# Kernel optimization log

Hardware: AMD Instinct MI355X
Metric: run time of the kernel (lower is better)

## Reference

```python
import jax, jax.numpy as jnp
import numpy as np

B, C, N, K = 2, 64, 20000, 16
COUT = 64


def setup_inputs() -> dict:
    key = jax.random.key(0)
    k1, k2, k3, k4, k5 = jax.random.split(key, 5)
    x = jax.random.normal(k1, (B, C, N, 1), dtype=jnp.float32)
    edge_index = jax.random.randint(k2, (2, B, N, K), 0, N)
    pos = jax.random.normal(k3, (B, 3, N, 1), dtype=jnp.float32)
    # BasicConv([2C, COUT]) -> 1x1 Conv2d weight [COUT, 2C] (+bias), then ReLU
    W = jax.random.normal(k4, (COUT, 2 * C), dtype=jnp.float32) * (1.0 / np.sqrt(2 * C))
    b = jax.random.normal(k5, (COUT,), dtype=jnp.float32) * 0.01
    return {"x": x, "edge_index": edge_index, "pos": pos, "W": W, "b": b}


def _gather(t, idx):
    # t: [B, C, N, 1], idx: [B, N, K] -> [B, C, N, K]
    t3 = t[..., 0]  # [B, C, N]
    return jax.vmap(lambda tb, ib: tb[:, ib])(t3, idx)


def reference(x, edge_index, pos, W, b):
    x_i = _gather(x, edge_index[1])           # [B, C, N, K] center
    x_j = _gather(x, edge_index[0])           # [B, C, N, K] neighbor
    feat = jnp.concatenate([x_i, x_j - x_i], axis=1)  # [B, 2C, N, K]
    # 1x1 conv + bias + ReLU
    out = jnp.einsum('oc,bcnk->bonk', W, feat) + b[None, :, None, None]
    out = jax.nn.relu(out)
    # distance-based suppression
    pos_i = _gather(pos, edge_index[1])       # [B, 3, N, K]
    pos_j = _gather(pos, edge_index[0])
    dis = jnp.sqrt(jnp.sum(jnp.square(pos_j - pos_i), axis=1))  # [B, N, K]
    suppression = 2.0 * jax.nn.sigmoid(-dis)[:, None, :, :]     # [B, 1, N, K]
    out = out * suppression
    max_value = jnp.max(out, axis=-1, keepdims=True)             # [B, COUT, N, 1]
    return max_value
```

## Files before the change

### kernel.cpp

```cpp
#include <hip/hip_runtime.h>
#include <math.h>

#define B_    2
#define C_    64
#define N_    20000
#define K_    16
#define COUT_ 64
#define TNC   64
#define NBC   ((N_ + TNC - 1) / TNC)
#define TN    16
#define NB    (N_ / TN)

typedef unsigned int   u32;
typedef unsigned short u16;
typedef __attribute__((ext_vector_type(8))) short bf16x8;
typedef __attribute__((ext_vector_type(4))) float f32x4;

static __device__ __forceinline__ u16 f2bf(float f) {
    union { float f; u32 u; } v; v.f = f;
    u32 r = (v.u + 0x7FFFu + ((v.u >> 16) & 1u)) >> 16;
    return (u16)r;
}
static __device__ __forceinline__ float uasf(u32 u) {
    union { u32 u; float f; } v; v.u = u; return v.f;
}
static __device__ __forceinline__ bf16x8 asbf(uint4 v) {
    union { uint4 u; bf16x8 b; } c; c.u = v; return c.b;
}

__global__ __launch_bounds__(256)
void precast(const float* __restrict__ x, const float* __restrict__ W,
             u16* __restrict__ xb, u16* __restrict__ wfrag) {
    const int bi = blockIdx.x;
    const int t  = threadIdx.x;

    if (bi == B_ * NBC) {
        const int l  = t & 63;
        const int ot = t >> 6;
        const int o  = ot * 16 + (l & 15);
        const int cb = (l >> 4) << 3;
        #pragma unroll
        for (int h = 0; h < 2; ++h) {
            u32 p1[4], p2[4];
            #pragma unroll
            for (int jj = 0; jj < 4; ++jj) {
                int c0 = h * 32 + cb + 2 * jj, c1 = c0 + 1;
                float w1a = W[o * 128 + c0],      w1b = W[o * 128 + c1];
                float w2a = W[o * 128 + 64 + c0], w2b = W[o * 128 + 64 + c1];
                p1[jj] = (u32)f2bf(w1a - w2a) | ((u32)f2bf(w1b - w2b) << 16);
                p2[jj] = (u32)f2bf(w2a)       | ((u32)f2bf(w2b)       << 16);
            }
            *(uint4*)&wfrag[(size_t)((ot * 4 + h)     * 64 + l) * 8] =
                make_uint4(p1[0], p1[1], p1[2], p1[3]);
            *(uint4*)&wfrag[(size_t)((ot * 4 + 2 + h) * 64 + l) * 8] =
                make_uint4(p2[0], p2[1], p2[2], p2[3]);
        }
        return;
    }

    __shared__ float tile[64][68];
    const int b  = bi / NBC;
    const int n0 = (bi % NBC) * TNC;
    const float* xbase = x + (size_t)b * C_ * N_;
    #pragma unroll
    for (int r = 0; r < 4; ++r) {
        int flat = r * 256 + t;
        int c = flat >> 4, ng = (flat & 15) * 4;
        int n = n0 + ng;
        float4 v;
        if (n + 3 < N_) {
            v = *(const float4*)&xbase[c * N_ + n];
        } else {
            v.x = (n     < N_) ? xbase[c * N_ + n    ] : 0.0f;
            v.y = (n + 1 < N_) ? xbase[c * N_ + n + 1] : 0.0f;
            v.z = (n + 2 < N_) ? xbase[c * N_ + n + 2] : 0.0f;
            v.w = (n + 3 < N_) ? xbase[c * N_ + n + 3] : 0.0f;
        }
        *(float4*)&tile[c][ng] = v;
    }
    __syncthreads();

    const int n = t >> 2, q = t & 3;
    if (n0 + n < N_) {
        u32 p[8];
        #pragma unroll
        for (int jj = 0; jj < 8; ++jj) {
            float v0 = tile[q * 16 + 2 * jj][n];
            float v1 = tile[q * 16 + 2 * jj + 1][n];
            p[jj] = (u32)f2bf(v0) | ((u32)f2bf(v1) << 16);
        }
        u16* dst = xb + ((size_t)(b * N_ + n0 + n)) * 64 + q * 16;
        *(uint4*)dst       = make_uint4(p[0], p[1], p[2], p[3]);
        *(uint4*)(dst + 8) = make_uint4(p[4], p[5], p[6], p[7]);
    }
}

__global__ __launch_bounds__(256)
void fused(const int* __restrict__ ei, const float* __restrict__ pos,
           const u16* __restrict__ xb, const u16* __restrict__ wfrag,
           const float* __restrict__ bias, float* __restrict__ out) {
    __shared__ uint2 esl[256];
    __shared__ float otile[16][66];

    const int bi   = blockIdx.x;
    const int b    = bi / NB;
    const int n0   = (bi % NB) * TN;
    const int t    = threadIdx.x;
    const int lane = t & 63;
    const int w    = t >> 6;
    const int g    = lane >> 4;
    const int col  = lane & 15;

    {
        const int idx = n0 * K_ + t;
        int i0 = ei[(size_t)b * N_ * K_ + idx];
        int i1 = ei[((size_t)B_ + b) * N_ * K_ + idx];
        const float* pb = pos + (size_t)b * 3 * N_;
        float dx = pb[i0]          - pb[i1];
        float dy = pb[N_ + i0]     - pb[N_ + i1];
        float dz = pb[2 * N_ + i0] - pb[2 * N_ + i1];
        float dis = sqrtf(dx * dx + dy * dy + dz * dz);
        float s = 2.0f / (1.0f + __expf(dis));
        esl[t] = make_uint2((u32)i0 | ((u32)i1 << 16), __float_as_uint(s));
    }

    bf16x8 wf[16];
    #pragma unroll
    for (int f = 0; f < 16; ++f)
        wf[f] = *(const bf16x8*)&wfrag[(size_t)(f * 64 + lane) * 8];
    const float bo0 = bias[col], bo1 = bias[16 + col],
                bo2 = bias[32 + col], bo3 = bias[48 + col];
    __syncthreads();

    const uint4* xrow = (const uint4*)(xb + (size_t)b * N_ * 64);

    #pragma unroll
    for (int it = 0; it < 4; ++it) {
        const int nt = it * 4 + w;
        uint2 ee = esl[nt * 16 + col];
        int   i0 = (int)(ee.x & 0xFFFFu);
        int   i1 = (int)(ee.x >> 16);
        const uint4* ri = xrow + ((size_t)i1 << 3);
        const uint4* rj = xrow + ((size_t)i0 << 3);
        bf16x8 xi_lo = asbf(ri[g]);
        bf16x8 xi_hi = asbf(ri[4 + g]);
        bf16x8 xj_lo = asbf(rj[g]);
        bf16x8 xj_hi = asbf(rj[4 + g]);

        f32x4 ac0 = {0,0,0,0}, ac1 = ac0, ac2 = ac0, ac3 = ac0;
        ac0 = __builtin_amdgcn_mfma_f32_16x16x32_bf16(xi_lo, wf[0],  ac0, 0,0,0);
        ac0 = __builtin_amdgcn_mfma_f32_16x16x32_bf16(xi_hi, wf[1],  ac0, 0,0,0);
        ac0 = __builtin_amdgcn_mfma_f32_16x16x32_bf16(xj_lo, wf[2],  ac0, 0,0,0);
        ac0 = __builtin_amdgcn_mfma_f32_16x16x32_bf16(xj_hi, wf[3],  ac0, 0,0,0);
        ac1 = __builtin_amdgcn_mfma_f32_16x16x32_bf16(xi_lo, wf[4],  ac1, 0,0,0);
        ac1 = __builtin_amdgcn_mfma_f32_16x16x32_bf16(xi_hi, wf[5],  ac1, 0,0,0);
        ac1 = __builtin_amdgcn_mfma_f32_16x16x32_bf16(xj_lo, wf[6],  ac1, 0,0,0);
        ac1 = __builtin_amdgcn_mfma_f32_16x16x32_bf16(xj_hi, wf[7],  ac1, 0,0,0);
        ac2 = __builtin_amdgcn_mfma_f32_16x16x32_bf16(xi_lo, wf[8],  ac2, 0,0,0);
        ac2 = __builtin_amdgcn_mfma_f32_16x16x32_bf16(xi_hi, wf[9],  ac2, 0,0,0);
        ac2 = __builtin_amdgcn_mfma_f32_16x16x32_bf16(xj_lo, wf[10], ac2, 0,0,0);
        ac2 = __builtin_amdgcn_mfma_f32_16x16x32_bf16(xj_hi, wf[11], ac2, 0,0,0);
        ac3 = __builtin_amdgcn_mfma_f32_16x16x32_bf16(xi_lo, wf[12], ac3, 0,0,0);
        ac3 = __builtin_amdgcn_mfma_f32_16x16x32_bf16(xi_hi, wf[13], ac3, 0,0,0);
        ac3 = __builtin_amdgcn_mfma_f32_16x16x32_bf16(xj_lo, wf[14], ac3, 0,0,0);
        ac3 = __builtin_amdgcn_mfma_f32_16x16x32_bf16(xj_hi, wf[15], ac3, 0,0,0);

        float m0 = 0.f, m1 = 0.f, m2 = 0.f, m3 = 0.f;
#define EPI(REG) { \
        float sv = uasf(esl[nt * 16 + g * 4 + REG].y); \
        m0 = fmaxf(m0, fmaxf(ac0[REG] + bo0, 0.f) * sv); \
        m1 = fmaxf(m1, fmaxf(ac1[REG] + bo1, 0.f) * sv); \
        m2 = fmaxf(m2, fmaxf(ac2[REG] + bo2, 0.f) * sv); \
        m3 = fmaxf(m3, fmaxf(ac3[REG] + bo3, 0.f) * sv); }
        EPI(0) EPI(1) EPI(2) EPI(3)
#undef EPI
        m0 = fmaxf(m0, __shfl_xor(m0, 16)); m0 = fmaxf(m0, __shfl_xor(m0, 32));
        m1 = fmaxf(m1, __shfl_xor(m1, 16)); m1 = fmaxf(m1, __shfl_xor(m1, 32));
        m2 = fmaxf(m2, __shfl_xor(m2, 16)); m2 = fmaxf(m2, __shfl_xor(m2, 32));
        m3 = fmaxf(m3, __shfl_xor(m3, 16)); m3 = fmaxf(m3, __shfl_xor(m3, 32));
        if (lane < 16) {
            otile[nt][col]      = m0;
            otile[nt][16 + col] = m1;
            otile[nt][32 + col] = m2;
            otile[nt][48 + col] = m3;
        }
    }
    __syncthreads();

    #pragma unroll
    for (int r = 0; r < 4; ++r) {
        int flat = r * 256 + t;
        int o = flat >> 4, n2 = flat & 15;
        __builtin_nontemporal_store(otile[n2][o],
            &out[((size_t)b * COUT_ + o) * N_ + n0 + n2]);
    }
}

extern "C" void kernel_launch(void* const* d_in, const int* in_sizes, int n_in,
                              void* d_out, int out_size, void* d_ws, size_t ws_size,
                              hipStream_t stream) {
    const float* x    = (const float*)d_in[0];
    const int*   ei   = (const int*)  d_in[1];
    const float* pos  = (const float*)d_in[2];
    const float* W    = (const float*)d_in[3];
    const float* bias = (const float*)d_in[4];
    float*       out  = (float*)d_out;

    u16* xb    = (u16*)d_ws;
    u16* wfrag = xb + (size_t)B_ * N_ * 64;

    hipLaunchKernelGGL(precast, dim3(B_ * NBC + 1), dim3(256), 0, stream,
                       x, W, xb, wfrag);
    hipLaunchKernelGGL(fused, dim3(B_ * NB), dim3(256), 0, stream,
                       ei, pos, xb, wfrag, bias, out);
}
```

Before: 110.7 us.

## Move edge index decode and distance suppression into prep kernel

The per-edge work (reading both edge index arrays, gathering positions, computing distance and sigmoid suppression) moves out of the fused kernel into the prep kernel. Prep now runs a fixed grid of 1024 blocks, and each block also handles a slice of edges. The packed index and suppression records go to a workspace buffer, which the fused kernel then reads with one 64-bit load per thread. This takes the dependent pos gathers off the MFMA kernel's critical path, at the cost of an extra 640 KB intermediate write and read.

New measurement: 118.1 us. +6.7%, slower.

```diff
diff --git a/kernel.cpp b/kernel.cpp
--- a/kernel.cpp
+++ b/kernel.cpp
@@ -10,9 +10,12 @@
 #define NBC   ((N_ + TNC - 1) / TNC)
 #define TN    16
 #define NB    (N_ / TN)
+#define NEDGE (B_ * N_ * K_)
+#define PREPB 1024
 
 typedef unsigned int   u32;
 typedef unsigned short u16;
+typedef unsigned long long u64;
 typedef __attribute__((ext_vector_type(8))) short bf16x8;
 typedef __attribute__((ext_vector_type(4))) float f32x4;
 
@@ -29,12 +32,34 @@
 }
 
 __global__ __launch_bounds__(256)
-void precast(const float* __restrict__ x, const float* __restrict__ W,
-             u16* __restrict__ xb, u16* __restrict__ wfrag) {
-    const int bi = blockIdx.x;
-    const int t  = threadIdx.x;
-
-    if (bi == B_ * NBC) {
+void prep(const float* __restrict__ x, const float* __restrict__ W,
+          const int* __restrict__ ei, const float* __restrict__ pos,
+          u16* __restrict__ xb, u16* __restrict__ wfrag,
+          u64* __restrict__ ebuf) {
+    const int bid = blockIdx.x;
+    const int t   = threadIdx.x;
+
+    {
+        const int base = bid * (NEDGE / PREPB);
+        #pragma unroll
+        for (int k = t; k < NEDGE / PREPB; k += 256) {
+            const int g = base + k;
+            const int b = g / (N_ * K_);
+            int i0 = __builtin_nontemporal_load(&ei[g]);
+            int i1 = __builtin_nontemporal_load(&ei[NEDGE + g]);
+            const float* pb = pos + (size_t)b * 3 * N_;
+            float dx = pb[i0]          - pb[i1];
+            float dy = pb[N_ + i0]     - pb[N_ + i1];
+            float dz = pb[2 * N_ + i0] - pb[2 * N_ + i1];
+            float dis = sqrtf(dx * dx + dy * dy + dz * dz);
+            float s = 2.0f / (1.0f + __expf(dis));
+            u64 rec = (u64)((u32)i0 | ((u32)i1 << 16)) |
+                      ((u64)__float_as_uint(s) << 32);
+            __builtin_nontemporal_store(rec, &ebuf[g]);
+        }
+    }
+
+    if (bid == B_ * NBC) {
         const int l  = t & 63;
         const int ot = t >> 6;
         const int o  = ot * 16 + (l & 15);
@@ -57,10 +82,11 @@
         }
         return;
     }
+    if (bid > B_ * NBC) return;
 
     __shared__ float tile[64][68];
-    const int b  = bi / NBC;
-    const int n0 = (bi % NBC) * TNC;
+    const int b  = bid / NBC;
+    const int n0 = (bid % NBC) * TNC;
     const float* xbase = x + (size_t)b * C_ * N_;
     #pragma unroll
     for (int r = 0; r < 4; ++r) {
@@ -96,9 +122,9 @@
 }
 
 __global__ __launch_bounds__(256)
-void fused(const int* __restrict__ ei, const float* __restrict__ pos,
-           const u16* __restrict__ xb, const u16* __restrict__ wfrag,
-           const float* __restrict__ bias, float* __restrict__ out) {
+void fused2(const u64* __restrict__ ebuf,
+            const u16* __restrict__ xb, const u16* __restrict__ wfrag,
+            const float* __restrict__ bias, float* __restrict__ out) {
     __shared__ uint2 esl[256];
     __shared__ float otile[16][66];
 
@@ -112,16 +138,9 @@
     const int col  = lane & 15;
 
     {
-        const int idx = n0 * K_ + t;
-        int i0 = ei[(size_t)b * N_ * K_ + idx];
-        int i1 = ei[((size_t)B_ + b) * N_ * K_ + idx];
-        const float* pb = pos + (size_t)b * 3 * N_;
-        float dx = pb[i0]          - pb[i1];
-        float dy = pb[N_ + i0]     - pb[N_ + i1];
-        float dz = pb[2 * N_ + i0] - pb[2 * N_ + i1];
-        float dis = sqrtf(dx * dx + dy * dy + dz * dz);
-        float s = 2.0f / (1.0f + __expf(dis));
-        esl[t] = make_uint2((u32)i0 | ((u32)i1 << 16), __float_as_uint(s));
+        u64 rec = __builtin_nontemporal_load(&ebuf[(size_t)b * N_ * K_ +
+                                                   n0 * K_ + t]);
+        esl[t] = make_uint2((u32)rec, (u32)(rec >> 32));
     }
 
     bf16x8 wf[16];
@@ -208,9 +227,10 @@
 
     u16* xb    = (u16*)d_ws;
     u16* wfrag = xb + (size_t)B_ * N_ * 64;
-
-    hipLaunchKernelGGL(precast, dim3(B_ * NBC + 1), dim3(256), 0, stream,
-                       x, W, xb, wfrag);
-    hipLaunchKernelGGL(fused, dim3(B_ * NB), dim3(256), 0, stream,
-                       ei, pos, xb, wfrag, bias, out);
-}
+    u64* ebuf  = (u64*)(wfrag + 64 * 64 * 2);
+
+    hipLaunchKernelGGL(prep, dim3(PREPB), dim3(256), 0, stream,
+                       x, W, ei, pos, xb, wfrag, ebuf);
+    hipLaunchKernelGGL(fused2, dim3(B_ * NB), dim3(256), 0, stream,
+                       ebuf, xb, wfrag, bias, out);
+}
```

## Stage weight fragments in LDS and issue all neighbor gathers upfront

Applied to the files above, without the earlier changes.

Weight fragments are copied into shared memory once per block and read from LDS for each MFMA, replacing the 16 per-lane register-held fragments. All 16 gather loads for the four node tiles are hoisted ahead of any compute, so more memory requests are in flight at once. Launch bounds now request 3 blocks per CU to limit register use. In exchange there are extra LDS reads per MFMA, a 16KB shared allocation per block that may limit occupancy, and higher register pressure from the hoisted loads.

New measurement: 108.1 us. 1.02x faster.

```diff
diff --git a/kernel.cpp b/kernel.cpp
--- a/kernel.cpp
+++ b/kernel.cpp
@@ -95,11 +95,12 @@
     }
 }
 
-__global__ __launch_bounds__(256)
+__global__ __launch_bounds__(256, 3)
 void fused(const int* __restrict__ ei, const float* __restrict__ pos,
            const u16* __restrict__ xb, const u16* __restrict__ wfrag,
            const float* __restrict__ bias, float* __restrict__ out) {
     __shared__ uint2 esl[256];
+    __shared__ u16   wlds[16 * 64 * 8];
     __shared__ float otile[16][66];
 
     const int bi   = blockIdx.x;
@@ -122,69 +123,83 @@
         float dis = sqrtf(dx * dx + dy * dy + dz * dz);
         float s = 2.0f / (1.0f + __expf(dis));
         esl[t] = make_uint2((u32)i0 | ((u32)i1 << 16), __float_as_uint(s));
-    }
-
-    bf16x8 wf[16];
-    #pragma unroll
-    for (int f = 0; f < 16; ++f)
-        wf[f] = *(const bf16x8*)&wfrag[(size_t)(f * 64 + lane) * 8];
+        #pragma unroll
+        for (int r = 0; r < 4; ++r) {
+            int e = r * 256 + t;
+            ((uint4*)wlds)[e] = ((const uint4*)wfrag)[e];
+        }
+    }
     const float bo0 = bias[col], bo1 = bias[16 + col],
                 bo2 = bias[32 + col], bo3 = bias[48 + col];
     __syncthreads();
 
     const uint4* xrow = (const uint4*)(xb + (size_t)b * N_ * 64);
 
-    #pragma unroll
-    for (int it = 0; it < 4; ++it) {
-        const int nt = it * 4 + w;
-        uint2 ee = esl[nt * 16 + col];
-        int   i0 = (int)(ee.x & 0xFFFFu);
-        int   i1 = (int)(ee.x >> 16);
-        const uint4* ri = xrow + ((size_t)i1 << 3);
-        const uint4* rj = xrow + ((size_t)i0 << 3);
-        bf16x8 xi_lo = asbf(ri[g]);
-        bf16x8 xi_hi = asbf(ri[4 + g]);
-        bf16x8 xj_lo = asbf(rj[g]);
-        bf16x8 xj_hi = asbf(rj[4 + g]);
-
-        f32x4 ac0 = {0,0,0,0}, ac1 = ac0, ac2 = ac0, ac3 = ac0;
-        ac0 = __builtin_amdgcn_mfma_f32_16x16x32_bf16(xi_lo, wf[0],  ac0, 0,0,0);
-        ac0 = __builtin_amdgcn_mfma_f32_16x16x32_bf16(xi_hi, wf[1],  ac0, 0,0,0);
-        ac0 = __builtin_amdgcn_mfma_f32_16x16x32_bf16(xj_lo, wf[2],  ac0, 0,0,0);
-        ac0 = __builtin_amdgcn_mfma_f32_16x16x32_bf16(xj_hi, wf[3],  ac0, 0,0,0);
-        ac1 = __builtin_amdgcn_mfma_f32_16x16x32_bf16(xi_lo, wf[4],  ac1, 0,0,0);
-        ac1 = __builtin_amdgcn_mfma_f32_16x16x32_bf16(xi_hi, wf[5],  ac1, 0,0,0);
-        ac1 = __builtin_amdgcn_mfma_f32_16x16x32_bf16(xj_lo, wf[6],  ac1, 0,0,0);
-        ac1 = __builtin_amdgcn_mfma_f32_16x16x32_bf16(xj_hi, wf[7],  ac1, 0,0,0);
-        ac2 = __builtin_amdgcn_mfma_f32_16x16x32_bf16(xi_lo, wf[8],  ac2, 0,0,0);
-        ac2 = __builtin_amdgcn_mfma_f32_16x16x32_bf16(xi_hi, wf[9],  ac2, 0,0,0);
-        ac2 = __builtin_amdgcn_mfma_f32_16x16x32_bf16(xj_lo, wf[10], ac2, 0,0,0);
-        ac2 = __builtin_amdgcn_mfma_f32_16x16x32_bf16(xj_hi, wf[11], ac2, 0,0,0);
-        ac3 = __builtin_amdgcn_mfma_f32_16x16x32_bf16(xi_lo, wf[12], ac3, 0,0,0);
-        ac3 = __builtin_amdgcn_mfma_f32_16x16x32_bf16(xi_hi, wf[13], ac3, 0,0,0);
-        ac3 = __builtin_amdgcn_mfma_f32_16x16x32_bf16(xj_lo, wf[14], ac3, 0,0,0);
-        ac3 = __builtin_amdgcn_mfma_f32_16x16x32_bf16(xj_hi, wf[15], ac3, 0,0,0);
-
-        float m0 = 0.f, m1 = 0.f, m2 = 0.f, m3 = 0.f;
-#define EPI(REG) { \
-        float sv = uasf(esl[nt * 16 + g * 4 + REG].y); \
-        m0 = fmaxf(m0, fmaxf(ac0[REG] + bo0, 0.f) * sv); \
-        m1 = fmaxf(m1, fmaxf(ac1[REG] + bo1, 0.f) * sv); \
-        m2 = fmaxf(m2, fmaxf(ac2[REG] + bo2, 0.f) * sv); \
-        m3 = fmaxf(m3, fmaxf(ac3[REG] + bo3, 0.f) * sv); }
-        EPI(0) EPI(1) EPI(2) EPI(3)
-#undef EPI
-        m0 = fmaxf(m0, __shfl_xor(m0, 16)); m0 = fmaxf(m0, __shfl_xor(m0, 32));
-        m1 = fmaxf(m1, __shfl_xor(m1, 16)); m1 = fmaxf(m1, __shfl_xor(m1, 32));
-        m2 = fmaxf(m2, __shfl_xor(m2, 16)); m2 = fmaxf(m2, __shfl_xor(m2, 32));
-        m3 = fmaxf(m3, __shfl_xor(m3, 16)); m3 = fmaxf(m3, __shfl_xor(m3, 32));
-        if (lane < 16) {
-            otile[nt][col]      = m0;
-            otile[nt][16 + col] = m1;
-            otile[nt][32 + col] = m2;
-            otile[nt][48 + col] = m3;
-        }
-    }
+    uint2 eA = esl[(w)      * 16 + col];
+    uint2 eB = esl[(4 + w)  * 16 + col];
+    uint2 eC = esl[(8 + w)  * 16 + col];
+    uint2 eD = esl[(12 + w) * 16 + col];
+    const uint4* riA = xrow + ((size_t)(eA.x >> 16) << 3);
+    const uint4* rjA = xrow + ((size_t)(eA.x & 0xFFFFu) << 3);
+    const uint4* riB = xrow + ((size_t)(eB.x >> 16) << 3);
+    const uint4* rjB = xrow + ((size_t)(eB.x & 0xFFFFu) << 3);
+    const uint4* riC = xrow + ((size_t)(eC.x >> 16) << 3);
+    const uint4* rjC = xrow + ((size_t)(eC.x & 0xFFFFu) << 3);
+    const uint4* riD = xrow + ((size_t)(eD.x >> 16) << 3);
+    const uint4* rjD = xrow + ((size_t)(eD.x & 0xFFFFu) << 3);
+
+    uint4 A0 = riA[g], A1 = riA[4 + g], A2 = rjA[g], A3 = rjA[4 + g];
+    uint4 B0 = riB[g], B1 = riB[4 + g], B2 = rjB[g], B3 = rjB[4 + g];
+    uint4 C0 = riC[g], C1 = riC[4 + g], C2 = rjC[g], C3 = rjC[4 + g];
+    uint4 D0 = riD[g], D1 = riD[4 + g], D2 = rjD[g], D3 = rjD[4 + g];
+
+#define WF(F) (*(const bf16x8*)&wlds[(size_t)((F) * 64 + lane) * 8])
+
+#define NODE(NT, L0, L1, L2, L3) { \
+    f32x4 ac0 = {0,0,0,0}, ac1 = ac0, ac2 = ac0, ac3 = ac0; \
+    bf16x8 f0 = asbf(L0), f1 = asbf(L1), f2 = asbf(L2), f3 = asbf(L3); \
+    ac0 = __builtin_amdgcn_mfma_f32_16x16x32_bf16(f0, WF(0),  ac0, 0,0,0); \
+    ac0 = __builtin_amdgcn_mfma_f32_16x16x32_bf16(f1, WF(1),  ac0, 0,0,0); \
+    ac0 = __builtin_amdgcn_mfma_f32_16x16x32_bf16(f2, WF(2),  ac0, 0,0,0); \
+    ac0 = __builtin_amdgcn_mfma_f32_16x16x32_bf16(f3, WF(3),  ac0, 0,0,0); \
+    ac1 = __builtin_amdgcn_mfma_f32_16x16x32_bf16(f0, WF(4),  ac1, 0,0,0); \
+    ac1 = __builtin_amdgcn_mfma_f32_16x16x32_bf16(f1, WF(5),  ac1, 0,0,0); \
+    ac1 = __builtin_amdgcn_mfma_f32_16x16x32_bf16(f2, WF(6),  ac1, 0,0,0); \
+    ac1 = __builtin_amdgcn_mfma_f32_16x16x32_bf16(f3, WF(7),  ac1, 0,0,0); \
+    ac2 = __builtin_amdgcn_mfma_f32_16x16x32_bf16(f0, WF(8),  ac2, 0,0,0); \
+    ac2 = __builtin_amdgcn_mfma_f32_16x16x32_bf16(f1, WF(9),  ac2, 0,0,0); \
+    ac2 = __builtin_amdgcn_mfma_f32_16x16x32_bf16(f2, WF(10), ac2, 0,0,0); \
+    ac2 = __builtin_amdgcn_mfma_f32_16x16x32_bf16(f3, WF(11), ac2, 0,0,0); \
+    ac3 = __builtin_amdgcn_mfma_f32_16x16x32_bf16(f0, WF(12), ac3, 0,0,0); \
+    ac3 = __builtin_amdgcn_mfma_f32_16x16x32_bf16(f1, WF(13), ac3, 0,0,0); \
+    ac3 = __builtin_amdgcn_mfma_f32_16x16x32_bf16(f2, WF(14), ac3, 0,0,0); \
+    ac3 = __builtin_amdgcn_mfma_f32_16x16x32_bf16(f3, WF(15), ac3, 0,0,0); \
+    float m0 = 0.f, m1 = 0.f, m2 = 0.f, m3 = 0.f; \
+    _Pragma("unroll") \
+    for (int r4 = 0; r4 < 4; ++r4) { \
+        float sv = uasf(esl[(NT) * 16 + g * 4 + r4].y); \
+        m0 = fmaxf(m0, fmaxf(ac0[r4] + bo0, 0.f) * sv); \
+        m1 = fmaxf(m1, fmaxf(ac1[r4] + bo1, 0.f) * sv); \
+        m2 = fmaxf(m2, fmaxf(ac2[r4] + bo2, 0.f) * sv); \
+        m3 = fmaxf(m3, fmaxf(ac3[r4] + bo3, 0.f) * sv); \
+    } \
+    m0 = fmaxf(m0, __shfl_xor(m0, 16)); m0 = fmaxf(m0, __shfl_xor(m0, 32)); \
+    m1 = fmaxf(m1, __shfl_xor(m1, 16)); m1 = fmaxf(m1, __shfl_xor(m1, 32)); \
+    m2 = fmaxf(m2, __shfl_xor(m2, 16)); m2 = fmaxf(m2, __shfl_xor(m2, 32)); \
+    m3 = fmaxf(m3, __shfl_xor(m3, 16)); m3 = fmaxf(m3, __shfl_xor(m3, 32)); \
+    if (lane < 16) { \
+        otile[NT][col]      = m0; \
+        otile[NT][16 + col] = m1; \
+        otile[NT][32 + col] = m2; \
+        otile[NT][48 + col] = m3; \
+    } }
+
+    NODE(w,      A0, A1, A2, A3)
+    NODE(4 + w,  B0, B1, B2, B3)
+    NODE(8 + w,  C0, C1, C2, C3)
+    NODE(12 + w, D0, D1, D2, D3)
+#undef NODE
+#undef WF
     __syncthreads();
 
     #pragma unroll
```

## Double-buffer gathered features into LDS via async global_load_lds

Applied to the files above, without the earlier changes.

Replaces direct register gathers of neighbor/center feature rows with asynchronous global-to-LDS loads, double-buffered per wave so the next tile's gather overlaps the current tile's MFMAs. Weight fragments and bias are staged in shared memory instead of held in 16 VGPR vectors, reducing register pressure. This adds roughly 40KB of LDS per block, which may reduce occupancy, and relies on hand-placed vmcnt waits for correctness.

Result: slower. 114.9 us (+3.8%).

```diff
diff --git a/kernel.cpp b/kernel.cpp
--- a/kernel.cpp
+++ b/kernel.cpp
@@ -16,6 +16,10 @@
 typedef __attribute__((ext_vector_type(8))) short bf16x8;
 typedef __attribute__((ext_vector_type(4))) float f32x4;
 
+typedef const __attribute__((address_space(1))) void* gas1_t;
+typedef __attribute__((address_space(3)))       void* las3_t;
+#define GL2LDS(g, l) __builtin_amdgcn_global_load_lds((gas1_t)(g), (las3_t)(l), 16, 0, 0)
+
 static __device__ __forceinline__ u16 f2bf(float f) {
     union { float f; u32 u; } v; v.f = f;
     u32 r = (v.u + 0x7FFFu + ((v.u >> 16) & 1u)) >> 16;
@@ -23,9 +27,6 @@
 }
 static __device__ __forceinline__ float uasf(u32 u) {
     union { u32 u; float f; } v; v.u = u; return v.f;
-}
-static __device__ __forceinline__ bf16x8 asbf(uint4 v) {
-    union { uint4 u; bf16x8 b; } c; c.u = v; return c.b;
 }
 
 __global__ __launch_bounds__(256)
@@ -99,7 +100,10 @@
 void fused(const int* __restrict__ ei, const float* __restrict__ pos,
            const u16* __restrict__ xb, const u16* __restrict__ wfrag,
            const float* __restrict__ bias, float* __restrict__ out) {
+    __shared__ u16   feat[4][2][4][512];
+    __shared__ u16   wlds[16 * 64 * 8];
     __shared__ uint2 esl[256];
+    __shared__ float bsl[64];
     __shared__ float otile[16][66];
 
     const int bi   = blockIdx.x;
@@ -122,58 +126,74 @@
         float dis = sqrtf(dx * dx + dy * dy + dz * dz);
         float s = 2.0f / (1.0f + __expf(dis));
         esl[t] = make_uint2((u32)i0 | ((u32)i1 << 16), __float_as_uint(s));
-    }
-
-    bf16x8 wf[16];
-    #pragma unroll
-    for (int f = 0; f < 16; ++f)
-        wf[f] = *(const bf16x8*)&wfrag[(size_t)(f * 64 + lane) * 8];
-    const float bo0 = bias[col], bo1 = bias[16 + col],
-                bo2 = bias[32 + col], bo3 = bias[48 + col];
+        #pragma unroll
+        for (int r = 0; r < 4; ++r) {
+            int e = r * 256 + t;
+            ((uint4*)wlds)[e] = ((const uint4*)wfrag)[e];
+        }
+        if (t < 64) bsl[t] = bias[t];
+    }
     __syncthreads();
 
-    const uint4* xrow = (const uint4*)(xb + (size_t)b * N_ * 64);
-
+    const u16* xbase = xb + (size_t)b * N_ * 64;
+
+    auto issue = [&](int nt, int bf) {
+        uint2 ee = esl[nt * 16 + col];
+        const u16* ri = xbase + ((size_t)(ee.x >> 16) << 6) + g * 8;
+        const u16* rj = xbase + ((size_t)(ee.x & 0xFFFFu) << 6) + g * 8;
+        GL2LDS(ri,      &feat[w][bf][0][0]);
+        GL2LDS(ri + 32, &feat[w][bf][1][0]);
+        GL2LDS(rj,      &feat[w][bf][2][0]);
+        GL2LDS(rj + 32, &feat[w][bf][3][0]);
+    };
+
+#define WF(F) (*(const bf16x8*)&wlds[(size_t)((F) * 64 + lane) * 8])
+
+    const float bo0 = bsl[col], bo1 = bsl[16 + col],
+                bo2 = bsl[32 + col], bo3 = bsl[48 + col];
+
+    issue(w, 0);
     #pragma unroll
     for (int it = 0; it < 4; ++it) {
         const int nt = it * 4 + w;
-        uint2 ee = esl[nt * 16 + col];
-        int   i0 = (int)(ee.x & 0xFFFFu);
-        int   i1 = (int)(ee.x >> 16);
-        const uint4* ri = xrow + ((size_t)i1 << 3);
-        const uint4* rj = xrow + ((size_t)i0 << 3);
-        bf16x8 xi_lo = asbf(ri[g]);
-        bf16x8 xi_hi = asbf(ri[4 + g]);
-        bf16x8 xj_lo = asbf(rj[g]);
-        bf16x8 xj_hi = asbf(rj[4 + g]);
+        const int bf = it & 1;
+        if (it < 3) issue((it + 1) * 4 + w, bf ^ 1);
+        if (it < 3) { asm volatile("s_waitcnt vmcnt(4)" ::: "memory"); }
+        else        { asm volatile("s_waitcnt vmcnt(0)" ::: "memory"); }
+        __builtin_amdgcn_sched_barrier(0);
+
+        bf16x8 f0 = *(const bf16x8*)&feat[w][bf][0][lane * 8];
+        bf16x8 f1 = *(const bf16x8*)&feat[w][bf][1][lane * 8];
+        bf16x8 f2 = *(const bf16x8*)&feat[w][bf][2][lane * 8];
+        bf16x8 f3 = *(const bf16x8*)&feat[w][bf][3][lane * 8];
 
         f32x4 ac0 = {0,0,0,0}, ac1 = ac0, ac2 = ac0, ac3 = ac0;
-        ac0 = __builtin_amdgcn_mfma_f32_16x16x32_bf16(xi_lo, wf[0],  ac0, 0,0,0);
-        ac0 = __builtin_amdgcn_mfma_f32_16x16x32_bf16(xi_hi, wf[1],  ac0, 0,0,0);
-        ac0 = __builtin_amdgcn_mfma_f32_16x16x32_bf16(xj_lo, wf[2],  ac0, 0,0,0);
-        ac0 = __builtin_amdgcn_mfma_f32_16x16x32_bf16(xj_hi, wf[3],  ac0, 0,0,0);
-        ac1 = __builtin_amdgcn_mfma_f32_16x16x32_bf16(xi_lo, wf[4],  ac1, 0,0,0);
-        ac1 = __builtin_amdgcn_mfma_f32_16x16x32_bf16(xi_hi, wf[5],  ac1, 0,0,0);
-        ac1 = __builtin_amdgcn_mfma_f32_16x16x32_bf16(xj_lo, wf[6],  ac1, 0,0,0);
-        ac1 = __builtin_amdgcn_mfma_f32_16x16x32_bf16(xj_hi, wf[7],  ac1, 0,0,0);
-        ac2 = __builtin_amdgcn_mfma_f32_16x16x32_bf16(xi_lo, wf[8],  ac2, 0,0,0);
-        ac2 = __builtin_amdgcn_mfma_f32_16x16x32_bf16(xi_hi, wf[9],  ac2, 0,0,0);
-        ac2 = __builtin_amdgcn_mfma_f32_16x16x32_bf16(xj_lo, wf[10], ac2, 0,0,0);
-        ac2 = __builtin_amdgcn_mfma_f32_16x16x32_bf16(xj_hi, wf[11], ac2, 0,0,0);
-        ac3 = __builtin_amdgcn_mfma_f32_16x16x32_bf16(xi_lo, wf[12], ac3, 0,0,0);
-        ac3 = __builtin_amdgcn_mfma_f32_16x16x32_bf16(xi_hi, wf[13], ac3, 0,0,0);
-        ac3 = __builtin_amdgcn_mfma_f32_16x16x32_bf16(xj_lo, wf[14], ac3, 0,0,0);
-        ac3 = __builtin_amdgcn_mfma_f32_16x16x32_bf16(xj_hi, wf[15], ac3, 0,0,0);
+        ac0 = __builtin_amdgcn_mfma_f32_16x16x32_bf16(f0, WF(0),  ac0, 0,0,0);
+        ac0 = __builtin_amdgcn_mfma_f32_16x16x32_bf16(f1, WF(1),  ac0, 0,0,0);
+        ac0 = __builtin_amdgcn_mfma_f32_16x16x32_bf16(f2, WF(2),  ac0, 0,0,0);
+        ac0 = __builtin_amdgcn_mfma_f32_16x16x32_bf16(f3, WF(3),  ac0, 0,0,0);
+        ac1 = __builtin_amdgcn_mfma_f32_16x16x32_bf16(f0, WF(4),  ac1, 0,0,0);
+        ac1 = __builtin_amdgcn_mfma_f32_16x16x32_bf16(f1, WF(5),  ac1, 0,0,0);
+        ac1 = __builtin_amdgcn_mfma_f32_16x16x32_bf16(f2, WF(6),  ac1, 0,0,0);
+        ac1 = __builtin_amdgcn_mfma_f32_16x16x32_bf16(f3, WF(7),  ac1, 0,0,0);
+        ac2 = __builtin_amdgcn_mfma_f32_16x16x32_bf16(f0, WF(8),  ac2, 0,0,0);
+        ac2 = __builtin_amdgcn_mfma_f32_16x16x32_bf16(f1, WF(9),  ac2, 0,0,0);
+        ac2 = __builtin_amdgcn_mfma_f32_16x16x32_bf16(f2, WF(10), ac2, 0,0,0);
+        ac2 = __builtin_amdgcn_mfma_f32_16x16x32_bf16(f3, WF(11), ac2, 0,0,0);
+        ac3 = __builtin_amdgcn_mfma_f32_16x16x32_bf16(f0, WF(12), ac3, 0,0,0);
+        ac3 = __builtin_amdgcn_mfma_f32_16x16x32_bf16(f1, WF(13), ac3, 0,0,0);
+        ac3 = __builtin_amdgcn_mfma_f32_16x16x32_bf16(f2, WF(14), ac3, 0,0,0);
+        ac3 = __builtin_amdgcn_mfma_f32_16x16x32_bf16(f3, WF(15), ac3, 0,0,0);
 
         float m0 = 0.f, m1 = 0.f, m2 = 0.f, m3 = 0.f;
-#define EPI(REG) { \
-        float sv = uasf(esl[nt * 16 + g * 4 + REG].y); \
-        m0 = fmaxf(m0, fmaxf(ac0[REG] + bo0, 0.f) * sv); \
-        m1 = fmaxf(m1, fmaxf(ac1[REG] + bo1, 0.f) * sv); \
-        m2 = fmaxf(m2, fmaxf(ac2[REG] + bo2, 0.f) * sv); \
-        m3 = fmaxf(m3, fmaxf(ac3[REG] + bo3, 0.f) * sv); }
-        EPI(0) EPI(1) EPI(2) EPI(3)
-#undef EPI
+        #pragma unroll
+        for (int r4 = 0; r4 < 4; ++r4) {
+            float sv = uasf(esl[nt * 16 + g * 4 + r4].y);
+            m0 = fmaxf(m0, fmaxf(ac0[r4] + bo0, 0.f) * sv);
+            m1 = fmaxf(m1, fmaxf(ac1[r4] + bo1, 0.f) * sv);
+            m2 = fmaxf(m2, fmaxf(ac2[r4] + bo2, 0.f) * sv);
+            m3 = fmaxf(m3, fmaxf(ac3[r4] + bo3, 0.f) * sv);
+        }
         m0 = fmaxf(m0, __shfl_xor(m0, 16)); m0 = fmaxf(m0, __shfl_xor(m0, 32));
         m1 = fmaxf(m1, __shfl_xor(m1, 16)); m1 = fmaxf(m1, __shfl_xor(m1, 32));
         m2 = fmaxf(m2, __shfl_xor(m2, 16)); m2 = fmaxf(m2, __shfl_xor(m2, 32));
@@ -185,6 +205,7 @@
             otile[nt][48 + col] = m3;
         }
     }
+#undef WF
     __syncthreads();
 
     #pragma unroll
```
